# Optimization experiments

Measured on AMD Instinct MI355X. Metric: run time of the kernel, lower is better.

## Reference

```python
import jax, jax.numpy as jnp
import numpy as np
import itertools

W_ASSIGN = 1.0   # options_file['assignments_loss_weight']
W_CAT = 0.5      # options_file['categorizer_loss_weight']


def _bce(p, y):
    # torch.nn.BCELoss semantics: log terms clamped at -100
    logp = jnp.clip(jnp.log(p), -100.0)
    log1mp = jnp.clip(jnp.log1p(-p), -100.0)
    return -(y * logp + (1.0 - y) * log1mp)


def setup_inputs() -> dict:
    key = jax.random.key(0)
    k0, k1, k2, k3 = jax.random.split(key, 4)
    B, P, M = 8192, 4, 12
    assignments = jax.random.uniform(k0, (B, P, M, M), dtype=jnp.float32)
    category = jax.random.uniform(k1, (B, P), dtype=jnp.float32)
    assignments_labels = jax.random.randint(k2, (B, P, M, M), 0, 2).astype(jnp.float32)
    category_labels = jax.random.randint(k3, (B, P), 0, 2).astype(jnp.float32)
    return {
        "assignments": assignments,
        "category": category,
        "assignments_labels": assignments_labels,
        "category_labels": category_labels,
    }


def reference(assignments, category, assignments_labels, category_labels):
    B, P = assignments.shape[0], assignments.shape[1]
    # All P! permutations, in itertools order (matches first-strict-min tie-break
    # of the original loop combined with argmin's first-occurrence rule).
    perms = jnp.asarray(np.array(list(itertools.permutations(range(P))), dtype=np.int32))  # [K, P]

    # [B, K, P, M, M]: assignments with slot dim permuted for every permutation
    permuted = assignments[:, perms]
    elem = _bce(permuted, assignments_labels[:, None])          # [B, K, P, M, M]
    per_perm_loss = elem.mean(axis=(2, 3, 4))                   # [B, K]

    min_loss = per_perm_loss.min(axis=1)                        # [B]
    best = jnp.argmin(per_perm_loss, axis=1)                    # [B]
    batch_perms = perms[best]                                   # [B, P]

    permuted_category = jnp.take_along_axis(category, batch_perms, axis=1)  # [B, P]

    assignments_loss = min_loss.mean()
    category_loss = _bce(permuted_category, category_labels).mean()
    return W_ASSIGN * assignments_loss + W_CAT * category_loss
```

## Files before the change

### kernel.cpp

```cpp
#include <hip/hip_runtime.h>
#include <math.h>


#define LOG2_CLIP (-144.26950408889634f)
#define LN2F      (0.6931471805599453f)

#define PK(a,b,c,d) ((unsigned)((4u*(a)) | ((16u+4u*(b))<<8) | \
                                ((32u+4u*(c))<<16) | ((48u+4u*(d))<<24)))
__device__ const unsigned PERM_PK[32] = {
    PK(0,1,2,3), PK(0,1,3,2), PK(0,2,1,3), PK(0,2,3,1), PK(0,3,1,2), PK(0,3,2,1),
    PK(1,0,2,3), PK(1,0,3,2), PK(1,2,0,3), PK(1,2,3,0), PK(1,3,0,2), PK(1,3,2,0),
    PK(2,0,1,3), PK(2,0,3,1), PK(2,1,0,3), PK(2,1,3,0), PK(2,3,0,1), PK(2,3,1,0),
    PK(3,0,1,2), PK(3,0,2,1), PK(3,1,0,2), PK(3,1,2,0), PK(3,2,0,1), PK(3,2,1,0),
    PK(0,1,2,3), PK(0,1,2,3), PK(0,1,2,3), PK(0,1,2,3),
    PK(0,1,2,3), PK(0,1,2,3), PK(0,1,2,3), PK(0,1,2,3)
};

__global__ __launch_bounds__(256) void hsl_partial(
    const float* __restrict__ assign,
    const float* __restrict__ cat,
    const float* __restrict__ alabels,
    const float* __restrict__ clabels,
    float* __restrict__ bsums)
{
    const int tid  = (int)threadIdx.x;
    const int wib  = tid >> 6;
    const int lane = tid & 63;
    const int b    = (int)blockIdx.x * 4 + wib;

    const float* __restrict__ A = assign  + (size_t)b * 576;
    const float* __restrict__ Y = alabels + (size_t)b * 576;

    float catv;
    {
        const int gq = (lane >> 2) & 3;
        const int gp = (lane >> 4) & 3;
        const float cq  = cat[(size_t)b * 4 + gq];
        const float cyp = clabels[(size_t)b * 4 + gp];
        catv = (cyp != 0.0f) ? fmaxf(__log2f(cq), LOG2_CLIP)
                             : fmaxf(__log2f(1.0f - cq), LOG2_CLIP);
    }

    float s[16], T[4];
#pragma unroll
    for (int i = 0; i < 16; ++i) s[i] = 0.0f;
#pragma unroll
    for (int i = 0; i < 4; ++i) T[i] = 0.0f;

#pragma unroll
    for (int it = 0; it < 3; ++it) {
        if (it < 2 || lane < 16) {
            const int e = lane + it * 64;
            float d[4], y[4];
#pragma unroll
            for (int q = 0; q < 4; ++q) {
                const float a  = A[q * 144 + e];
                const float la = fmaxf(__log2f(a),        LOG2_CLIP);
                const float lb = fmaxf(__log2f(1.0f - a), LOG2_CLIP);
                d[q] = la - lb;
                T[q] += lb;
            }
#pragma unroll
            for (int p = 0; p < 4; ++p) y[p] = Y[p * 144 + e];
#pragma unroll
            for (int p = 0; p < 4; ++p)
#pragma unroll
                for (int q = 0; q < 4; ++q)
                    s[p * 4 + q] = fmaf(y[p], d[q], s[p * 4 + q]);
        }
    }
#pragma unroll
    for (int i = 0; i < 16; ++i) s[i] += T[i & 3];

    const bool h32 = (lane & 32) != 0;
    const bool h16 = (lane & 16) != 0;
    const bool h8  = (lane & 8)  != 0;
    const bool h4  = (lane & 4)  != 0;

    float t[8];
#pragma unroll
    for (int i = 0; i < 8; ++i) {
        const float keep = h32 ? s[i + 8] : s[i];
        const float send = h32 ? s[i]     : s[i + 8];
        t[i] = keep + __shfl_xor(send, 32, 64);
    }
    float u[4];
#pragma unroll
    for (int i = 0; i < 4; ++i) {
        const float keep = h16 ? t[i + 4] : t[i];
        const float send = h16 ? t[i]     : t[i + 4];
        u[i] = keep + __shfl_xor(send, 16, 64);
    }
    float w[2];
#pragma unroll
    for (int i = 0; i < 2; ++i) {
        const float keep = h8 ? u[i + 2] : u[i];
        const float send = h8 ? u[i]     : u[i + 2];
        w[i] = keep + __shfl_xor(send, 8, 64);
    }
    float x;
    {
        const float keep = h4 ? w[1] : w[0];
        const float send = h4 ? w[0] : w[1];
        x = keep + __shfl_xor(send, 4, 64);
    }
    x += __shfl_xor(x, 2, 64);
    x += __shfl_xor(x, 1, 64);

    unsigned pk = PERM_PK[lane & 31];
    const int a0 = (int)( pk        & 0xFFu);
    const int a1 = (int)((pk >> 8)  & 0xFFu);
    const int a2 = (int)((pk >> 16) & 0xFFu);
    const int a3 = (int)( pk >> 24        );
    const float v0 = __shfl(x, a0, 64);
    const float v1 = __shfl(x, a1, 64);
    const float v2 = __shfl(x, a2, 64);
    const float v3 = __shfl(x, a3, 64);
    const float c0 = __shfl(catv, a0, 64);
    const float c1 = __shfl(catv, a1, 64);
    const float c2 = __shfl(catv, a2, 64);
    const float c3 = __shfl(catv, a3, 64);
    float score = (v0 + v1) + (v2 + v3);
    float csum  = (c0 + c1) + (c2 + c3);
    if (lane >= 24) score = -__builtin_huge_valf();

#pragma unroll
    for (int m = 16; m >= 1; m >>= 1) {
        const float os = __shfl_xor(score, m, 64);
        const float oc = __shfl_xor(csum,  m, 64);
        const bool take = os > score;
        score = take ? os : score;
        csum  = take ? oc : csum;
    }

    if (lane == 0) {
        bsums[(size_t)blockIdx.x * 4 + wib] =
            -LN2F * (score * (1.0f / 576.0f) + 0.125f * csum);
    }
}

__global__ __launch_bounds__(256) void hsl_reduce(
    const float* __restrict__ bsums,
    float* __restrict__ out,
    int n, int B)
{
    __shared__ double sw[4];
    const int tid  = (int)threadIdx.x;
    const int wid  = tid >> 6;
    const int lane = tid & 63;

    const float4* __restrict__ v4 = (const float4*)bsums;
    const int n4 = n >> 2;
    double d = 0.0;
    for (int i = tid; i < n4; i += 256) {
        const float4 v = v4[i];
        d += (double)((v.x + v.y) + (v.z + v.w));
    }

#pragma unroll
    for (int m = 32; m >= 1; m >>= 1)
        d += __shfl_xor(d, m, 64);

    if (lane == 0) sw[wid] = d;
    __syncthreads();

    if (tid == 0) {
        const double t = (sw[0] + sw[1]) + (sw[2] + sw[3]);
        out[0] = (float)(t / (double)B);
    }
}

extern "C" void kernel_launch(void* const* d_in, const int* in_sizes, int n_in,
                              void* d_out, int out_size, void* d_ws, size_t ws_size,
                              hipStream_t stream) {
    const float* assign  = (const float*)d_in[0];
    const float* cat     = (const float*)d_in[1];
    const float* alabels = (const float*)d_in[2];
    const float* clabels = (const float*)d_in[3];
    float* out = (float*)d_out;

    const int B = in_sizes[0] / 576;
    float* bsums = (float*)d_ws;

    const int nblocks = B / 4;
    hipLaunchKernelGGL(hsl_partial, dim3(nblocks), dim3(256), 0, stream,
                       assign, cat, alabels, clabels, bsums);
    hipLaunchKernelGGL(hsl_reduce, dim3(1), dim3(256), 0, stream,
                       bsums, out, B , B);
}
```

Baseline: 15.74 us.

## Use permlane swaps, DPP and ballot-based argmin in per-batch wave reduction

Replaces the first two butterfly shuffle stages with permlane32/16 swap intrinsics and the last two with DPP row operations, avoiding LDS-backed shuffles. The argmin with category payload becomes a plain max reduction followed by a ballot to find the first winning lane and readlane gathers of the category logs. It also pre-sums the four waves' results per block through shared memory, so the final reduce kernel reads a quarter as many values. This adds a block barrier and depends on first-lane tie-breaking matching the original.

```diff
diff --git a/kernel.cpp b/kernel.cpp
--- a/kernel.cpp
+++ b/kernel.cpp
@@ -4,6 +4,27 @@
 
 #define LOG2_CLIP (-144.26950408889634f)
 #define LN2F      (0.6931471805599453f)
+
+typedef int v2i __attribute__((ext_vector_type(2)));
+
+__device__ __forceinline__ float pl32_add(float a, float b) {
+    v2i r = __builtin_amdgcn_permlane32_swap(__float_as_int(a),
+                                             __float_as_int(b), false, false);
+    return __int_as_float(r[0]) + __int_as_float(r[1]);
+}
+__device__ __forceinline__ float pl16_add(float a, float b) {
+    v2i r = __builtin_amdgcn_permlane16_swap(__float_as_int(a),
+                                             __float_as_int(b), false, false);
+    return __int_as_float(r[0]) + __int_as_float(r[1]);
+}
+__device__ __forceinline__ float dpp_x1(float x) {
+    return __int_as_float(__builtin_amdgcn_update_dpp(
+        0, __float_as_int(x), 0xB1, 0xF, 0xF, false));
+}
+__device__ __forceinline__ float dpp_x2(float x) {
+    return __int_as_float(__builtin_amdgcn_update_dpp(
+        0, __float_as_int(x), 0x4E, 0xF, 0xF, false));
+}
 
 #define PK(a,b,c,d) ((unsigned)((4u*(a)) | ((16u+4u*(b))<<8) | \
                                 ((32u+4u*(c))<<16) | ((48u+4u*(d))<<24)))
@@ -23,6 +44,8 @@
     const float* __restrict__ clabels,
     float* __restrict__ bsums)
 {
+    __shared__ float lred[4];
+
     const int tid  = (int)threadIdx.x;
     const int wib  = tid >> 6;
     const int lane = tid & 63;
@@ -31,14 +54,16 @@
     const float* __restrict__ A = assign  + (size_t)b * 576;
     const float* __restrict__ Y = alabels + (size_t)b * 576;
 
+    const unsigned pk = PERM_PK[lane & 31];
+
     float catv;
     {
-        const int gq = (lane >> 2) & 3;
-        const int gp = (lane >> 4) & 3;
+        const int gq = lane & 3;
+        const int gp = (lane >> 2) & 3;
         const float cq  = cat[(size_t)b * 4 + gq];
         const float cyp = clabels[(size_t)b * 4 + gp];
-        catv = (cyp != 0.0f) ? fmaxf(__log2f(cq), LOG2_CLIP)
-                             : fmaxf(__log2f(1.0f - cq), LOG2_CLIP);
+        const float arg = (cyp != 0.0f) ? cq : 1.0f - cq;
+        catv = fmaxf(__log2f(arg), LOG2_CLIP);
     }
 
     float s[16], T[4];
@@ -72,25 +97,15 @@
 #pragma unroll
     for (int i = 0; i < 16; ++i) s[i] += T[i & 3];
 
-    const bool h32 = (lane & 32) != 0;
-    const bool h16 = (lane & 16) != 0;
-    const bool h8  = (lane & 8)  != 0;
-    const bool h4  = (lane & 4)  != 0;
-
     float t[8];
 #pragma unroll
-    for (int i = 0; i < 8; ++i) {
-        const float keep = h32 ? s[i + 8] : s[i];
-        const float send = h32 ? s[i]     : s[i + 8];
-        t[i] = keep + __shfl_xor(send, 32, 64);
-    }
+    for (int i = 0; i < 8; ++i) t[i] = pl32_add(s[i], s[i + 8]);
     float u[4];
 #pragma unroll
-    for (int i = 0; i < 4; ++i) {
-        const float keep = h16 ? t[i + 4] : t[i];
-        const float send = h16 ? t[i]     : t[i + 4];
-        u[i] = keep + __shfl_xor(send, 16, 64);
-    }
+    for (int i = 0; i < 4; ++i) u[i] = pl16_add(t[i], t[i + 4]);
+
+    const bool h8 = (lane & 8) != 0;
+    const bool h4 = (lane & 4) != 0;
     float w[2];
 #pragma unroll
     for (int i = 0; i < 2; ++i) {
@@ -104,10 +119,9 @@
         const float send = h4 ? w[0] : w[1];
         x = keep + __shfl_xor(send, 4, 64);
     }
-    x += __shfl_xor(x, 2, 64);
-    x += __shfl_xor(x, 1, 64);
-
-    unsigned pk = PERM_PK[lane & 31];
+    x += dpp_x2(x);
+    x += dpp_x1(x);
+
     const int a0 = (int)( pk        & 0xFFu);
     const int a1 = (int)((pk >> 8)  & 0xFFu);
     const int a2 = (int)((pk >> 16) & 0xFFu);
@@ -116,26 +130,37 @@
     const float v1 = __shfl(x, a1, 64);
     const float v2 = __shfl(x, a2, 64);
     const float v3 = __shfl(x, a3, 64);
-    const float c0 = __shfl(catv, a0, 64);
-    const float c1 = __shfl(catv, a1, 64);
-    const float c2 = __shfl(catv, a2, 64);
-    const float c3 = __shfl(catv, a3, 64);
     float score = (v0 + v1) + (v2 + v3);
-    float csum  = (c0 + c1) + (c2 + c3);
     if (lane >= 24) score = -__builtin_huge_valf();
 
-#pragma unroll
-    for (int m = 16; m >= 1; m >>= 1) {
-        const float os = __shfl_xor(score, m, 64);
-        const float oc = __shfl_xor(csum,  m, 64);
-        const bool take = os > score;
-        score = take ? os : score;
-        csum  = take ? oc : csum;
-    }
+    float smax = score;
+    smax = fmaxf(smax, __shfl_xor(smax, 16, 64));
+    smax = fmaxf(smax, __shfl_xor(smax, 8, 64));
+    smax = fmaxf(smax, __shfl_xor(smax, 4, 64));
+    smax = fmaxf(smax, dpp_x2(smax));
+    smax = fmaxf(smax, dpp_x1(smax));
+
+    const unsigned long long bal = __ballot(score == smax);
+    const int win = (int)__builtin_ctzll(bal);
+    const unsigned pkw = (unsigned)__builtin_amdgcn_readlane((int)pk, win);
+
+    const int c0 = (int)((pkw >> 2)  & 0x0Fu);
+    const int c1 = (int)((pkw >> 10) & 0x0Fu);
+    const int c2 = (int)((pkw >> 18) & 0x0Fu);
+    const int c3 = (int)((pkw >> 26) & 0x0Fu);
+    const float g0 = __int_as_float(__builtin_amdgcn_readlane(__float_as_int(catv), c0));
+    const float g1 = __int_as_float(__builtin_amdgcn_readlane(__float_as_int(catv), c1));
+    const float g2 = __int_as_float(__builtin_amdgcn_readlane(__float_as_int(catv), c2));
+    const float g3 = __int_as_float(__builtin_amdgcn_readlane(__float_as_int(catv), c3));
+    const float csum = (g0 + g1) + (g2 + g3);
 
     if (lane == 0) {
-        bsums[(size_t)blockIdx.x * 4 + wib] =
-            -LN2F * (score * (1.0f / 576.0f) + 0.125f * csum);
+        lred[wib] = -LN2F * (smax * (1.0f / 576.0f) + 0.125f * csum);
+    }
+    __syncthreads();
+
+    if (tid == 0) {
+        bsums[blockIdx.x] = (lred[0] + lred[1]) + (lred[2] + lred[3]);
     }
 }
 
@@ -186,5 +211,5 @@
     hipLaunchKernelGGL(hsl_partial, dim3(nblocks), dim3(256), 0, stream,
                        assign, cat, alabels, clabels, bsums);
     hipLaunchKernelGGL(hsl_reduce, dim3(1), dim3(256), 0, stream,
-                       bsums, out, B , B);
-}
+                       bsums, out, nblocks, B);
+}
```

Result: faster. 13.81 us, median of 2 (-12.3%).
